# Kernel optimization log

Measured on AMD Instinct MI355X. Metric: run time of the kernel, lower is better.

The kernel has to match this reference:

```python
import jax, jax.numpy as jnp
import numpy as np

B, NL, C, H, W = 4, 2048, 128, 128, 128
N_PTS0, N_PTS1 = 32, 8
SCALE = N_PTS0 // N_PTS1  # MaxPool1d kernel/stride
FEATURE_DIM = 5
BN_EPS = 1e-5


def setup_inputs() -> dict:
    key = jax.random.key(0)
    ks = jax.random.split(key, 12)
    fm = jax.random.normal(ks[0], (B, C, H, W), dtype=jnp.float32)
    lines = jax.random.uniform(ks[1], (B, NL, 2, 2), dtype=jnp.float32) * 128.0
    P = C // 2
    s = 0.05
    return {
        "feature_map": fm,
        "lines": lines,
        # Bottleneck1D params (BatchNorm in eval mode: running_mean=0, running_var=1)
        "bn1_g": jnp.ones((C,), jnp.float32), "bn1_b": jnp.zeros((C,), jnp.float32),
        "conv1_w": jax.random.normal(ks[2], (P, C, 1), jnp.float32) * s,
        "conv1_b": jnp.zeros((P,), jnp.float32),
        "bn2_g": jnp.ones((P,), jnp.float32), "bn2_b": jnp.zeros((P,), jnp.float32),
        "conv2_w": jax.random.normal(ks[3], (P, P, 3), jnp.float32) * s,
        "conv2_b": jnp.zeros((P,), jnp.float32),
        "bn3_g": jnp.ones((P,), jnp.float32), "bn3_b": jnp.zeros((P,), jnp.float32),
        "conv3_w": jax.random.normal(ks[4], (C, P, 1), jnp.float32) * s,
        "conv3_b": jnp.zeros((C,), jnp.float32),
        # fc2: ReLU -> Linear(dim_loi*n_pts1 + 5, 4)
        "fc2_w": jax.random.normal(ks[5], (4, C * N_PTS1 + FEATURE_DIM), jnp.float32) * s,
        "fc2_b": jnp.zeros((4,), jnp.float32),
    }


def _bn(x, g, b):
    # eval-mode BatchNorm1d with running_mean=0, running_var=1
    return x * (g / jnp.sqrt(1.0 + BN_EPS))[None, :, None] + b[None, :, None]


def _conv1d(x, w, b, pad):
    y = jax.lax.conv_general_dilated(x, w, (1,), [(pad, pad)],
                                     dimension_numbers=("NCH", "OIH", "NCH"))
    return y + b[None, :, None]


def _loi_gather(fm, lines):
    # sample points along each line: [B, NL, N_PTS0, 2]
    lam = jnp.linspace(0.0, 1.0, N_PTS0, dtype=jnp.float32)[None, None, :, None]
    p = lines[:, :, 0:1, :] * lam + lines[:, :, 1:2, :] * (1.0 - lam) - 0.5
    p = p.reshape(B, -1, 2)                      # [B, NL*N_PTS0, 2]
    px, py = p[..., 0], p[..., 1]
    px0 = jnp.clip(jnp.floor(px), 0.0, 127.0)
    py0 = jnp.clip(jnp.floor(py), 0.0, 127.0)
    px1 = jnp.clip(px0 + 1.0, 0.0, 127.0)
    py1 = jnp.clip(py0 + 1.0, 0.0, 127.0)
    px0l, py0l = px0.astype(jnp.int32), py0.astype(jnp.int32)
    px1l, py1l = px1.astype(jnp.int32), py1.astype(jnp.int32)

    gather = jax.vmap(lambda f, yi, xi: f[:, yi, xi])  # [C, P] per image
    # weights exactly as in the torch source
    xp = (gather(fm, py0l, px0l) * ((px1 - px) * (py1 - py))[:, None, :]
          + gather(fm, py1l, px0l) * ((px - px0) * (py1 - py))[:, None, :]
          + gather(fm, py0l, px1l) * ((px1 - px) * (py - py0))[:, None, :]
          + gather(fm, py1l, px1l) * ((px - px0) * (py - py0))[:, None, :])
    # [B, C, NL*N_PTS0] -> [B*NL, C, N_PTS0]
    xp = xp.reshape(B, C, NL, N_PTS0).transpose(0, 2, 1, 3).reshape(B * NL, C, N_PTS0)
    return xp


def reference(feature_map, lines, bn1_g, bn1_b, conv1_w, conv1_b,
              bn2_g, bn2_b, conv2_w, conv2_b, bn3_g, bn3_b,
              conv3_w, conv3_b, fc2_w, fc2_b):
    xp = _loi_gather(feature_map, lines)               # [B*NL, C, N_PTS0]
    # MaxPool1d(SCALE, SCALE)
    x = xp.reshape(B * NL, C, N_PTS1, SCALE).max(axis=-1)
    # Bottleneck1D residual block
    y = jax.nn.relu(_bn(x, bn1_g, bn1_b))
    y = _conv1d(y, conv1_w, conv1_b, 0)
    y = jax.nn.relu(_bn(y, bn2_g, bn2_b))
    y = _conv1d(y, conv2_w, conv2_b, 1)
    y = jax.nn.relu(_bn(y, bn3_g, bn3_b))
    y = _conv1d(y, conv3_w, conv3_b, 0)
    x = x + y                                          # [B*NL, C, N_PTS1]
    # line geometry feature (use_cood=1, use_slop=1)
    xyu, xyv = lines[:, :, 0, :], lines[:, :, 1, :]
    u2v = jnp.sqrt(((xyu - xyv) ** 2).sum(-1, keepdims=True)).clip(min=1e-6)
    f = jnp.concatenate([xyu / 128.0, xyv / 128.0, u2v], axis=-1)
    f = f.reshape(B * NL, FEATURE_DIM)
    # concat + fc2 (ReLU -> Linear)
    x = jnp.concatenate([x.reshape(B * NL, C * N_PTS1), f], axis=1)
    logits = jax.nn.relu(x) @ fc2_w.T + fc2_b
    prob = jax.nn.softmax(logits, axis=1)
    return logits, prob
```

## Files before the change

kernel.cpp:

```cpp
#include <hip/hip_runtime.h>
#include <math.h>

#define BB 4
#define NLL 2048
#define CC 128
#define HH 128
#define WW 128
#define NPTS0 32
#define NPTS1 8
#define PP 64
#define FDIM 5
#define FCK (CC*NPTS1 + FDIM)
#define FCKP 1032

typedef __attribute__((ext_vector_type(8))) short bf16x8;
typedef __attribute__((ext_vector_type(4))) float f32x4;

__device__ __forceinline__ unsigned short f2bf(float f) {
    union { float f; unsigned u; } v; v.f = f;
    unsigned u = v.u;
    return (unsigned short)((u + 0x7fffu + ((u >> 16) & 1u)) >> 16);
}
__device__ __forceinline__ float bf2f(unsigned short s) {
    union { unsigned u; float f; } v; v.u = ((unsigned)s) << 16;
    return v.f;
}

__global__ __launch_bounds__(256)
void transpose_prep(const float* __restrict__ fm, const float* __restrict__ w1,
                    const float* __restrict__ w2, const float* __restrict__ w3,
                    const float* __restrict__ fcw,
                    unsigned short* __restrict__ fmT,
                    unsigned short* __restrict__ W1b,
                    unsigned short* __restrict__ W2b,
                    unsigned short* __restrict__ W3b,
                    float* __restrict__ fcwP) {
    const int t = threadIdx.x;
    if (blockIdx.x >= 512) {
        int gid = (blockIdx.x - 512) * 256 + t;
        for (int e = gid; e < 32800; e += 4096) {
            if (e < 8192) {
                W1b[e] = f2bf(w1[e]);
            } else if (e < 20480) {
                int g = e - 8192;
                int tt = g >> 12, r = g & 4095;
                int p = r >> 6, q = r & 63;
                W2b[tt * 4096 + p * 64 + q] = f2bf(w2[p * 192 + q * 3 + tt]);
            } else if (e < 28672) {
                int g = e - 20480;
                W3b[g] = f2bf(w3[g]);
            } else {
                int g = e - 28672;
                int o = g / FCKP, r = g - o * FCKP;
                fcwP[g] = (r < FCK) ? fcw[o * FCK + r] : 0.0f;
            }
        }
        return;
    }
    __shared__ unsigned short tile[2][128 * 72];
    const int by = blockIdx.x;
    const int b = by >> 7, y = by & 127;
    const float* src = fm + ((size_t)b * CC) * (HH * WW) + (size_t)y * WW;
    const int x4 = (t & 31) * 4;
    const int xh = x4 >> 6, xl = x4 & 63;
    #pragma unroll
    for (int i = 0; i < 16; ++i) {
        int r = (t >> 5) + 8 * i;
        float4 v = *(const float4*)&src[(size_t)r * (HH * WW) + x4];
        ushort4 u;
        u.x = f2bf(v.x); u.y = f2bf(v.y); u.z = f2bf(v.z); u.w = f2bf(v.w);
        *(ushort4*)&tile[xh][r * 72 + (xl ^ (r & 28))] = u;
    }
    __syncthreads();
    const int c4 = (t & 31) * 4;
    #pragma unroll
    for (int h = 0; h < 2; ++h) {
        unsigned short* dst = fmT + ((size_t)by * WW + h * 64) * CC;
        #pragma unroll
        for (int i = 0; i < 8; ++i) {
            int x = (t >> 5) + 8 * i;
            ushort4 u;
            u.x = tile[h][(c4 + 0) * 72 + (x ^ ((c4 + 0) & 28))];
            u.y = tile[h][(c4 + 1) * 72 + (x ^ ((c4 + 1) & 28))];
            u.z = tile[h][(c4 + 2) * 72 + (x ^ ((c4 + 2) & 28))];
            u.w = tile[h][(c4 + 3) * 72 + (x ^ ((c4 + 3) & 28))];
            *(ushort4*)&dst[(size_t)x * CC + c4] = u;
        }
    }
}

__global__ __launch_bounds__(256, 6)
void line_mfma(const unsigned short* __restrict__ fmT,
               const float* __restrict__ lines,
               const float* __restrict__ bn1_g, const float* __restrict__ bn1_b,
               const unsigned short* __restrict__ W1b, const float* __restrict__ b1,
               const float* __restrict__ bn2_g, const float* __restrict__ bn2_b,
               const unsigned short* __restrict__ W2b, const float* __restrict__ b2,
               const float* __restrict__ bn3_g, const float* __restrict__ bn3_b,
               const unsigned short* __restrict__ W3b, const float* __restrict__ b3,
               const float* __restrict__ fcwP,  const float* __restrict__ fcb,
               float* __restrict__ out) {
    __shared__ unsigned short s_xs[32 * 136];
    __shared__ unsigned short s_z1[4 * 10 * 72];
    __shared__ unsigned short s_z2[32 * 72];
    __shared__ float s_red[4 * 8];

    const int bx  = blockIdx.x;
    const int L0  = bx * 4;
    const int b   = bx >> 9;
    const int tid = threadIdx.x;
    const int lane = tid & 63;
    const int wv   = tid >> 6;
    const int quad = lane >> 4;
    const int l16  = lane & 15;
    const float inv_s = 1.0f / sqrtf(1.0f + 1e-5f);

    {
        int m = tid >> 3;
        int line = m >> 3, k = m & 7;
        int c16 = (tid & 7) * 16;
        const float* ln = lines + (size_t)(L0 + line) * 4;
        float lx0 = ln[0], ly0 = ln[1], lx1 = ln[2], ly1 = ln[3];
        const unsigned short* base = fmT + (size_t)b * (HH * WW * CC) + c16;
        float acc[16];
        #pragma unroll
        for (int i = 0; i < 16; ++i) acc[i] = -INFINITY;
        #pragma unroll
        for (int j = 0; j < 4; ++j) {
            int pt = k * 4 + j;
            float lam = (float)pt * (1.0f / 31.0f);
            float om  = 1.0f - lam;
            float px = lx0 * lam + lx1 * om - 0.5f;
            float py = ly0 * lam + ly1 * om - 0.5f;
            float px0 = fminf(fmaxf(floorf(px), 0.0f), 127.0f);
            float py0 = fminf(fmaxf(floorf(py), 0.0f), 127.0f);
            float px1 = fminf(px0 + 1.0f, 127.0f);
            float py1 = fminf(py0 + 1.0f, 127.0f);
            int ix0 = (int)px0, ix1 = (int)px1, iy0 = (int)py0, iy1 = (int)py1;
            float ax = px1 - px, bxv = px - px0, ay = py1 - py, byv = py - py0;
            float wA = ax * ay, wB = bxv * ay, wC = ax * byv, wD = bxv * byv;
            int oA = (iy0 * WW + ix0) * CC, oB = (iy1 * WW + ix0) * CC;
            int oC = (iy0 * WW + ix1) * CC, oD = (iy1 * WW + ix1) * CC;
            bf16x8 a0 = *(const bf16x8*)(base + oA);
            bf16x8 a1 = *(const bf16x8*)(base + oA + 8);
            bf16x8 b0 = *(const bf16x8*)(base + oB);
            bf16x8 b1v = *(const bf16x8*)(base + oB + 8);
            bf16x8 c0 = *(const bf16x8*)(base + oC);
            bf16x8 c1 = *(const bf16x8*)(base + oC + 8);
            bf16x8 d0 = *(const bf16x8*)(base + oD);
            bf16x8 d1 = *(const bf16x8*)(base + oD + 8);
            #pragma unroll
            for (int i = 0; i < 8; ++i) {
                float v = wA * bf2f((unsigned short)a0[i])
                        + wB * bf2f((unsigned short)b0[i])
                        + wC * bf2f((unsigned short)c0[i])
                        + wD * bf2f((unsigned short)d0[i]);
                acc[i] = fmaxf(acc[i], v);
                float v2 = wA * bf2f((unsigned short)a1[i])
                         + wB * bf2f((unsigned short)b1v[i])
                         + wC * bf2f((unsigned short)c1[i])
                         + wD * bf2f((unsigned short)d1[i]);
                acc[8 + i] = fmaxf(acc[8 + i], v2);
            }
        }
        bf16x8 lo, hi;
        #pragma unroll
        for (int i = 0; i < 8; ++i) {
            lo[i] = (short)f2bf(acc[i]);
            hi[i] = (short)f2bf(acc[8 + i]);
        }
        *(bf16x8*)&s_xs[m * 136 + c16]     = lo;
        *(bf16x8*)&s_xs[m * 136 + c16 + 8] = hi;
    }
    __syncthreads();

    {
        int mh = wv & 1, nh = wv >> 1;
        int mrow = mh * 16 + l16;
        bf16x8 afr[4];
        #pragma unroll
        for (int kc = 0; kc < 4; ++kc) {
            bf16x8 x = *(const bf16x8*)&s_xs[mrow * 136 + kc * 32 + quad * 8];
            int c0 = kc * 32 + quad * 8;
            float4 g0 = *(const float4*)(bn1_g + c0);
            float4 g1 = *(const float4*)(bn1_g + c0 + 4);
            float4 bb0 = *(const float4*)(bn1_b + c0);
            float4 bb1 = *(const float4*)(bn1_b + c0 + 4);
            float gs[8] = {g0.x, g0.y, g0.z, g0.w, g1.x, g1.y, g1.z, g1.w};
            float bs[8] = {bb0.x, bb0.y, bb0.z, bb0.w, bb1.x, bb1.y, bb1.z, bb1.w};
            bf16x8 pk;
            #pragma unroll
            for (int i = 0; i < 8; ++i) {
                float v = fmaxf(bf2f((unsigned short)x[i]) * (gs[i] * inv_s) + bs[i], 0.0f);
                pk[i] = (short)f2bf(v);
            }
            afr[kc] = pk;
        }
        #pragma unroll
        for (int sub = 0; sub < 2; ++sub) {
            int p = nh * 32 + sub * 16 + l16;
            f32x4 acc = {0.f, 0.f, 0.f, 0.f};
            #pragma unroll
            for (int kc = 0; kc < 4; ++kc) {
                bf16x8 bf = *(const bf16x8*)(W1b + p * 128 + kc * 32 + quad * 8);
                acc = __builtin_amdgcn_mfma_f32_16x16x32_bf16(afr[kc], bf, acc, 0, 0, 0);
            }
            float s2 = bn2_g[p] * inv_s, bb2 = bn2_b[p], cb = b1[p];
            #pragma unroll
            for (int r = 0; r < 4; ++r) {
                int mm = mh * 16 + quad * 4 + r;
                int lline = mm >> 3, kk = mm & 7;
                float v = fmaxf((acc[r] + cb) * s2 + bb2, 0.0f);
                s_z1[lline * 720 + (kk + 1) * 72 + p] = f2bf(v);
            }
        }
        #pragma unroll
        for (int e = tid; e < 512; e += 256) {
            int lline = e >> 7;
            int rr = (e >> 6) & 1;
            int q = e & 63;
            s_z1[lline * 720 + (rr ? 9 : 0) * 72 + q] = 0;
        }
    }
    __syncthreads();

    {
        int mh = wv & 1, nh = wv >> 1;
        int mrow = mh * 16 + l16;
        int linea = mrow >> 3, ka = mrow & 7;
        const unsigned short* arow = s_z1 + linea * 720 + ka * 72;
        bf16x8 afr[3][2];
        #pragma unroll
        for (int t = 0; t < 3; ++t)
            #pragma unroll
            for (int kc = 0; kc < 2; ++kc)
                afr[t][kc] = *(const bf16x8*)&arow[t * 72 + kc * 32 + quad * 8];
        #pragma unroll
        for (int sub = 0; sub < 2; ++sub) {
            int p = nh * 32 + sub * 16 + l16;
            f32x4 acc = {0.f, 0.f, 0.f, 0.f};
            #pragma unroll
            for (int t = 0; t < 3; ++t) {
                #pragma unroll
                for (int kc = 0; kc < 2; ++kc) {
                    bf16x8 bf = *(const bf16x8*)(W2b + t * 4096 + p * 64 + kc * 32 + quad * 8);
                    acc = __builtin_amdgcn_mfma_f32_16x16x32_bf16(afr[t][kc], bf, acc, 0, 0, 0);
                }
            }
            float s3 = bn3_g[p] * inv_s, bb3 = bn3_b[p], cb = b2[p];
            #pragma unroll
            for (int r = 0; r < 4; ++r) {
                int mm = mh * 16 + quad * 4 + r;
                float v = fmaxf((acc[r] + cb) * s3 + bb3, 0.0f);
                s_z2[mm * 72 + p] = f2bf(v);
            }
        }
    }
    __syncthreads();

    float p0 = 0.f, p1 = 0.f, p2 = 0.f, p3 = 0.f;
    {
        int mh = wv & 1;
        int n0 = (wv >> 1) * 64;
        int mrow = mh * 16 + l16;
        bf16x8 a0 = *(const bf16x8*)&s_z2[mrow * 72 + quad * 8];
        bf16x8 a1 = *(const bf16x8*)&s_z2[mrow * 72 + 32 + quad * 8];
        int kbase = (quad & 1) * 4;
        #pragma unroll
        for (int sub = 0; sub < 4; ++sub) {
            int c = n0 + sub * 16 + l16;
            f32x4 acc = {0.f, 0.f, 0.f, 0.f};
            bf16x8 bf0 = *(const bf16x8*)(W3b + c * 64 + quad * 8);
            bf16x8 bf1 = *(const bf16x8*)(W3b + c * 64 + 32 + quad * 8);
            acc = __builtin_amdgcn_mfma_f32_16x16x32_bf16(a0, bf0, acc, 0, 0, 0);
            acc = __builtin_amdgcn_mfma_f32_16x16x32_bf16(a1, bf1, acc, 0, 0, 0);
            float cb = b3[c];
            int idx = c * 8 + kbase;
            float4 w0 = *(const float4*)(fcwP + 0 * FCKP + idx);
            float4 w1v = *(const float4*)(fcwP + 1 * FCKP + idx);
            float4 w2v = *(const float4*)(fcwP + 2 * FCKP + idx);
            float4 w3v = *(const float4*)(fcwP + 3 * FCKP + idx);
            const float* w0a = (const float*)&w0;
            const float* w1a = (const float*)&w1v;
            const float* w2a = (const float*)&w2v;
            const float* w3a = (const float*)&w3v;
            #pragma unroll
            for (int r = 0; r < 4; ++r) {
                int mm = mh * 16 + quad * 4 + r;
                float xv = bf2f(s_xs[mm * 136 + c]);
                float v = fmaxf(xv + acc[r] + cb, 0.0f);
                p0 = fmaf(v, w0a[r], p0);
                p1 = fmaf(v, w1a[r], p1);
                p2 = fmaf(v, w2a[r], p2);
                p3 = fmaf(v, w3a[r], p3);
            }
        }
    }
    #pragma unroll
    for (int off = 16; off >= 1; off >>= 1) {
        p0 += __shfl_down(p0, off);
        p1 += __shfl_down(p1, off);
        p2 += __shfl_down(p2, off);
        p3 += __shfl_down(p3, off);
    }
    if ((lane & 31) == 0) {
        int h = lane >> 5;
        s_red[wv * 8 + h * 4 + 0] = p0;
        s_red[wv * 8 + h * 4 + 1] = p1;
        s_red[wv * 8 + h * 4 + 2] = p2;
        s_red[wv * 8 + h * 4 + 3] = p3;
    }
    __syncthreads();

    if (tid < 4) {
        int line = tid;
        int wa = line >> 1;
        int h  = (line & 1) * 4;
        float lg[4];
        #pragma unroll
        for (int o = 0; o < 4; ++o)
            lg[o] = fcb[o] + s_red[wa * 8 + h + o] + s_red[(wa + 2) * 8 + h + o];
        const float* ln = lines + (size_t)(L0 + line) * 4;
        float ux = ln[0], uy = ln[1], vx = ln[2], vy = ln[3];
        float dx = ux - vx, dy = uy - vy;
        float d = fmaxf(sqrtf(dx * dx + dy * dy), 1e-6f);
        float ft[FDIM] = {ux * (1.0f / 128.0f), uy * (1.0f / 128.0f),
                          vx * (1.0f / 128.0f), vy * (1.0f / 128.0f), d};
        #pragma unroll
        for (int j = 0; j < FDIM; ++j) {
            float fv = fmaxf(ft[j], 0.0f);
            #pragma unroll
            for (int o = 0; o < 4; ++o)
                lg[o] = fmaf(fv, fcwP[o * FCKP + 1024 + j], lg[o]);
        }
        float m = fmaxf(fmaxf(lg[0], lg[1]), fmaxf(lg[2], lg[3]));
        float e0 = expf(lg[0] - m), e1 = expf(lg[1] - m);
        float e2 = expf(lg[2] - m), e3 = expf(lg[3] - m);
        float inv = 1.0f / (e0 + e1 + e2 + e3);
        float* lo = out + (size_t)(L0 + line) * 4;
        lo[0] = lg[0]; lo[1] = lg[1]; lo[2] = lg[2]; lo[3] = lg[3];
        float* pr = out + (size_t)BB * NLL * 4 + (size_t)(L0 + line) * 4;
        pr[0] = e0 * inv; pr[1] = e1 * inv; pr[2] = e2 * inv; pr[3] = e3 * inv;
    }
}

__global__ __launch_bounds__(256)
void transpose_fm2(const float* __restrict__ fm, float* __restrict__ fmT) {
    __shared__ float tile[32 * 132];
    const int c0 = blockIdx.x * 32;
    const int by = blockIdx.y;
    const int b = by >> 7, y = by & 127;
    const int t = threadIdx.x;
    const float* src = fm + ((size_t)b * CC) * (HH * WW) + (size_t)y * WW;
    const int x4 = (t & 31) * 4;
    #pragma unroll
    for (int i = 0; i < 4; ++i) {
        int r = (t >> 5) + 8 * i;
        *(float4*)&tile[r * 132 + x4] =
            *(const float4*)&src[(size_t)(c0 + r) * (HH * WW) + x4];
    }
    __syncthreads();
    float* dst = fmT + (size_t)by * WW * CC + c0 + (t & 31);
    const int cr = (t & 31) * 132;
    #pragma unroll
    for (int i = 0; i < 16; ++i) {
        int x = (t >> 5) + 8 * i;
        dst[(size_t)x * CC] = tile[cr + x];
    }
}

template<bool TRANS>
__global__ __launch_bounds__(256)
void line_kernel_v1(const float* __restrict__ fm,
                    const float* __restrict__ lines,
                    const float* __restrict__ bn1_g, const float* __restrict__ bn1_b,
                    const float* __restrict__ w1,    const float* __restrict__ b1,
                    const float* __restrict__ bn2_g, const float* __restrict__ bn2_b,
                    const float* __restrict__ w2,    const float* __restrict__ b2,
                    const float* __restrict__ bn3_g, const float* __restrict__ bn3_b,
                    const float* __restrict__ w3,    const float* __restrict__ b3,
                    const float* __restrict__ fcw,   const float* __restrict__ fcb,
                    float* __restrict__ out) {
    __shared__ int   s_ix0[32], s_ix1[32], s_iy0[32], s_iy1[32];
    __shared__ float s_wA[32], s_wB[32], s_wC[32], s_wD[32];
    __shared__ float xs [8][132];
    __shared__ float ybn[8][132];
    __shared__ float z1 [64][12];
    __shared__ float z2 [64][8];
    __shared__ float s_feat[8];
    __shared__ float s_red[16];

    const int L   = blockIdx.x;
    const int b   = L / NLL;
    const int tid = threadIdx.x;
    const float inv_s = 1.0f / sqrtf(1.0f + 1e-5f);
    const float* ln = lines + (size_t)L * 4;

    if (tid < 32) {
        float lam = (float)tid * (1.0f / 31.0f);
        float om  = 1.0f - lam;
        float px = ln[0] * lam + ln[2] * om - 0.5f;
        float py = ln[1] * lam + ln[3] * om - 0.5f;
        float px0 = fminf(fmaxf(floorf(px), 0.0f), 127.0f);
        float py0 = fminf(fmaxf(floorf(py), 0.0f), 127.0f);
        float px1 = fminf(px0 + 1.0f, 127.0f);
        float py1 = fminf(py0 + 1.0f, 127.0f);
        s_ix0[tid] = (int)px0; s_ix1[tid] = (int)px1;
        s_iy0[tid] = (int)py0; s_iy1[tid] = (int)py1;
        float ax = px1 - px, bxv = px - px0, ay = py1 - py, byv = py - py0;
        s_wA[tid] = ax  * ay;  s_wB[tid] = bxv * ay;
        s_wC[tid] = ax  * byv; s_wD[tid] = bxv * byv;
    }
    if (tid == 0) {
        float ux = ln[0], uy = ln[1], vx = ln[2], vy = ln[3];
        float dx = ux - vx, dy = uy - vy;
        float d = fmaxf(sqrtf(dx * dx + dy * dy), 1e-6f);
        s_feat[0] = ux / 128.0f; s_feat[1] = uy / 128.0f;
        s_feat[2] = vx / 128.0f; s_feat[3] = vy / 128.0f;
        s_feat[4] = d;
    }
    __syncthreads();
    {
        int cq = tid & 31, k = tid >> 5, c0 = cq * 4;
        float4 acc;
        acc.x = -INFINITY; acc.y = -INFINITY; acc.z = -INFINITY; acc.w = -INFINITY;
        #pragma unroll
        for (int j = 0; j < 4; ++j) {
            int pt = k * 4 + j;
            int ix0 = s_ix0[pt], ix1 = s_ix1[pt];
            int iy0 = s_iy0[pt], iy1 = s_iy1[pt];
            float wA = s_wA[pt], wB = s_wB[pt], wC = s_wC[pt], wD = s_wD[pt];
            float4 vA, vB, vC, vD;
            if (TRANS) {
                const float* base = fm + (size_t)b * HH * WW * CC;
                vA = *(const float4*)(base + ((size_t)(iy0 * WW + ix0)) * CC + c0);
                vB = *(const float4*)(base + ((size_t)(iy1 * WW + ix0)) * CC + c0);
                vC = *(const float4*)(base + ((size_t)(iy0 * WW + ix1)) * CC + c0);
                vD = *(const float4*)(base + ((size_t)(iy1 * WW + ix1)) * CC + c0);
            } else {
                const float* base = fm + ((size_t)b * CC + c0) * HH * WW;
                int oA = iy0 * WW + ix0, oB = iy1 * WW + ix0;
                int oC = iy0 * WW + ix1, oD = iy1 * WW + ix1;
                vA.x = base[oA];           vB.x = base[oB];
                vC.x = base[oC];           vD.x = base[oD];
                vA.y = base[HH*WW + oA];   vB.y = base[HH*WW + oB];
                vC.y = base[HH*WW + oC];   vD.y = base[HH*WW + oD];
                vA.z = base[2*HH*WW + oA]; vB.z = base[2*HH*WW + oB];
                vC.z = base[2*HH*WW + oC]; vD.z = base[2*HH*WW + oD];
                vA.w = base[3*HH*WW + oA]; vB.w = base[3*HH*WW + oB];
                vC.w = base[3*HH*WW + oC]; vD.w = base[3*HH*WW + oD];
            }
            float4 v;
            v.x = wA * vA.x + wB * vB.x + wC * vC.x + wD * vD.x;
            v.y = wA * vA.y + wB * vB.y + wC * vC.y + wD * vD.y;
            v.z = wA * vA.z + wB * vB.z + wC * vC.z + wD * vD.z;
            v.w = wA * vA.w + wB * vB.w + wC * vC.w + wD * vD.w;
            acc.x = fmaxf(acc.x, v.x); acc.y = fmaxf(acc.y, v.y);
            acc.z = fmaxf(acc.z, v.z); acc.w = fmaxf(acc.w, v.w);
        }
        *(float4*)(&xs[k][c0]) = acc;
    }
    __syncthreads();
    for (int e = tid; e < 1024; e += 256) {
        int k = e >> 7, c = e & 127;
        ybn[k][c] = fmaxf(xs[k][c] * (bn1_g[c] * inv_s) + bn1_b[c], 0.0f);
    }
    __syncthreads();
    if (tid < 64) { z1[tid][0] = 0.0f; z1[tid][9] = 0.0f; }
    {
        int p = tid >> 2, kq = tid & 3;
        const float* wrow = w1 + p * 128;
        float a0a = 0.f, a0b = 0.f, a1a = 0.f, a1b = 0.f;
        #pragma unroll 8
        for (int c = 0; c < 128; c += 4) {
            float4 w  = *(const float4*)(wrow + c);
            float4 ya = *(const float4*)(&ybn[kq][c]);
            float4 yb = *(const float4*)(&ybn[kq + 4][c]);
            a0a = fmaf(w.x, ya.x, a0a); a0b = fmaf(w.y, ya.y, a0b);
            a0a = fmaf(w.z, ya.z, a0a); a0b = fmaf(w.w, ya.w, a0b);
            a1a = fmaf(w.x, yb.x, a1a); a1b = fmaf(w.y, yb.y, a1b);
            a1a = fmaf(w.z, yb.z, a1a); a1b = fmaf(w.w, yb.w, a1b);
        }
        float s2 = bn2_g[p] * inv_s, bb = bn2_b[p], cb = b1[p];
        z1[p][1 + kq]     = fmaxf((a0a + a0b + cb) * s2 + bb, 0.0f);
        z1[p][1 + kq + 4] = fmaxf((a1a + a1b + cb) * s2 + bb, 0.0f);
    }
    __syncthreads();
    {
        int p = tid >> 2, kq = tid & 3;
        const float* wrow = w2 + p * 192;
        float acc0 = 0.f, acc1 = 0.f;
        #pragma unroll 4
        for (int q = 0; q < 64; ++q) {
            float w0 = wrow[q * 3 + 0], w1v = wrow[q * 3 + 1], w2v = wrow[q * 3 + 2];
            const float* zr = &z1[q][0];
            acc0 = fmaf(w0, zr[kq], acc0);
            acc0 = fmaf(w1v, zr[kq + 1], acc0);
            acc0 = fmaf(w2v, zr[kq + 2], acc0);
            acc1 = fmaf(w0, zr[kq + 4], acc1);
            acc1 = fmaf(w1v, zr[kq + 5], acc1);
            acc1 = fmaf(w2v, zr[kq + 6], acc1);
        }
        float s3 = bn3_g[p] * inv_s, bb = bn3_b[p], cb = b2[p];
        z2[p][kq]     = fmaxf((acc0 + cb) * s3 + bb, 0.0f);
        z2[p][kq + 4] = fmaxf((acc1 + cb) * s3 + bb, 0.0f);
    }
    __syncthreads();
    float part0 = 0.f, part1 = 0.f, part2 = 0.f, part3 = 0.f;
    {
        int c = tid >> 1, kq = tid & 1;
        const float* wrow = w3 + c * 64;
        float acc[4] = {0.f, 0.f, 0.f, 0.f};
        #pragma unroll 8
        for (int q = 0; q < 64; ++q) {
            float w = wrow[q];
            acc[0] = fmaf(w, z2[q][kq], acc[0]);
            acc[1] = fmaf(w, z2[q][kq + 2], acc[1]);
            acc[2] = fmaf(w, z2[q][kq + 4], acc[2]);
            acc[3] = fmaf(w, z2[q][kq + 6], acc[3]);
        }
        float cb = b3[c];
        #pragma unroll
        for (int i = 0; i < 4; ++i) {
            int k = kq + 2 * i;
            float v = fmaxf(xs[k][c] + acc[i] + cb, 0.0f);
            int idx = c * 8 + k;
            part0 = fmaf(v, fcw[0 * FCK + idx], part0);
            part1 = fmaf(v, fcw[1 * FCK + idx], part1);
            part2 = fmaf(v, fcw[2 * FCK + idx], part2);
            part3 = fmaf(v, fcw[3 * FCK + idx], part3);
        }
    }
    #pragma unroll
    for (int off = 32; off > 0; off >>= 1) {
        part0 += __shfl_down(part0, off);
        part1 += __shfl_down(part1, off);
        part2 += __shfl_down(part2, off);
        part3 += __shfl_down(part3, off);
    }
    if ((tid & 63) == 0) {
        int w = tid >> 6;
        s_red[w * 4 + 0] = part0; s_red[w * 4 + 1] = part1;
        s_red[w * 4 + 2] = part2; s_red[w * 4 + 3] = part3;
    }
    __syncthreads();
    if (tid == 0) {
        float lg[4];
        #pragma unroll
        for (int o = 0; o < 4; ++o)
            lg[o] = fcb[o] + s_red[o] + s_red[4 + o] + s_red[8 + o] + s_red[12 + o];
        #pragma unroll
        for (int j = 0; j < FDIM; ++j) {
            float fv = fmaxf(s_feat[j], 0.0f);
            #pragma unroll
            for (int o = 0; o < 4; ++o)
                lg[o] = fmaf(fv, fcw[o * FCK + 1024 + j], lg[o]);
        }
        float m = fmaxf(fmaxf(lg[0], lg[1]), fmaxf(lg[2], lg[3]));
        float e0 = expf(lg[0] - m), e1 = expf(lg[1] - m);
        float e2 = expf(lg[2] - m), e3 = expf(lg[3] - m);
        float inv = 1.0f / (e0 + e1 + e2 + e3);
        float* lo = out + (size_t)L * 4;
        lo[0] = lg[0]; lo[1] = lg[1]; lo[2] = lg[2]; lo[3] = lg[3];
        float* pr = out + (size_t)BB * NLL * 4 + (size_t)L * 4;
        pr[0] = e0 * inv; pr[1] = e1 * inv; pr[2] = e2 * inv; pr[3] = e3 * inv;
    }
}

extern "C" void kernel_launch(void* const* d_in, const int* in_sizes, int n_in,
                              void* d_out, int out_size, void* d_ws, size_t ws_size,
                              hipStream_t stream) {
    const float* fm     = (const float*)d_in[0];
    const float* lines  = (const float*)d_in[1];
    const float* bn1_g  = (const float*)d_in[2];
    const float* bn1_b  = (const float*)d_in[3];
    const float* w1     = (const float*)d_in[4];
    const float* b1     = (const float*)d_in[5];
    const float* bn2_g  = (const float*)d_in[6];
    const float* bn2_b  = (const float*)d_in[7];
    const float* w2     = (const float*)d_in[8];
    const float* b2     = (const float*)d_in[9];
    const float* bn3_g  = (const float*)d_in[10];
    const float* bn3_b  = (const float*)d_in[11];
    const float* w3     = (const float*)d_in[12];
    const float* b3     = (const float*)d_in[13];
    const float* fcw    = (const float*)d_in[14];
    const float* fcb    = (const float*)d_in[15];
    float* out = (float*)d_out;

    const size_t fmTb_bytes = (size_t)BB * HH * WW * CC * sizeof(unsigned short);
    const size_t fmTf_bytes = (size_t)BB * HH * WW * CC * sizeof(float);
    const size_t wb_bytes   = 57344;
    const size_t fcwP_bytes = 4 * FCKP * sizeof(float);

    if (ws_size >= fmTb_bytes + wb_bytes + fcwP_bytes) {
        unsigned short* fmT = (unsigned short*)d_ws;
        unsigned short* W1b = (unsigned short*)((char*)d_ws + fmTb_bytes);
        unsigned short* W2b = W1b + 8192;
        unsigned short* W3b = W2b + 12288;
        float* fcwP = (float*)((char*)d_ws + fmTb_bytes + wb_bytes);
        transpose_prep<<<512 + 16, 256, 0, stream>>>(
            fm, w1, w2, w3, fcw, fmT, W1b, W2b, W3b, fcwP);
        line_mfma<<<BB * NLL / 4, 256, 0, stream>>>(
            fmT, lines, bn1_g, bn1_b, W1b, b1, bn2_g, bn2_b, W2b, b2,
            bn3_g, bn3_b, W3b, b3, fcwP, fcb, out);
    } else if (ws_size >= fmTf_bytes) {
        float* fmT = (float*)d_ws;
        dim3 tg(CC / 32, BB * HH);
        transpose_fm2<<<tg, 256, 0, stream>>>(fm, fmT);
        line_kernel_v1<true><<<BB * NLL, 256, 0, stream>>>(
            fmT, lines, bn1_g, bn1_b, w1, b1, bn2_g, bn2_b, w2, b2,
            bn3_g, bn3_b, w3, b3, fcw, fcb, out);
    } else {
        line_kernel_v1<false><<<BB * NLL, 256, 0, stream>>>(
            fm, lines, bn1_g, bn1_b, w1, b1, bn2_g, bn2_b, w2, b2,
            bn3_g, bn3_b, w3, b3, fcw, fcb, out);
    }
}
```

Baseline: 177.1 us.

## Precompute bilinear offsets in LDS, halve gather width, alias shared buffers for occupancy

The first 128 threads compute bilinear corner offsets and weights once per sample point and store them in shared memory. Every thread then gathers 8 channels per pass over two passes, instead of 16 channels with all coordinate math repeated. The shared buffers are packed into one aliased byte array, and the launch bound goes from 6 to 8 blocks per CU. The aim is lower register pressure and higher occupancy, hiding gather latency better. In exchange it adds an extra barrier and LDS traffic, and it serializes the gather into two passes.

```diff
diff --git a/kernel.cpp b/kernel.cpp
--- a/kernel.cpp
+++ b/kernel.cpp
@@ -89,7 +89,7 @@
     }
 }
 
-__global__ __launch_bounds__(256, 6)
+__global__ __launch_bounds__(256, 8)
 void line_mfma(const unsigned short* __restrict__ fmT,
                const float* __restrict__ lines,
                const float* __restrict__ bn1_g, const float* __restrict__ bn1_b,
@@ -100,10 +100,19 @@
                const unsigned short* __restrict__ W3b, const float* __restrict__ b3,
                const float* __restrict__ fcwP,  const float* __restrict__ fcb,
                float* __restrict__ out) {
-    __shared__ unsigned short s_xs[32 * 136];
-    __shared__ unsigned short s_z1[4 * 10 * 72];
-    __shared__ unsigned short s_z2[32 * 72];
-    __shared__ float s_red[4 * 8];
+    __shared__ __align__(16) char smem[19200];
+    int*   s_oA = (int*)(smem + 0);
+    int*   s_oB = (int*)(smem + 512);
+    int*   s_oC = (int*)(smem + 1024);
+    int*   s_oD = (int*)(smem + 1536);
+    float* s_wA = (float*)(smem + 2048);
+    float* s_wB = (float*)(smem + 2560);
+    float* s_wC = (float*)(smem + 3072);
+    float* s_wD = (float*)(smem + 3584);
+    unsigned short* s_z1 = (unsigned short*)(smem + 0);
+    unsigned short* s_xs = (unsigned short*)(smem + 5760);
+    unsigned short* s_z2 = (unsigned short*)(smem + 14464);
+    float* s_red = (float*)(smem + 19072);
 
     const int bx  = blockIdx.x;
     const int L0  = bx * 4;
@@ -115,62 +124,60 @@
     const int l16  = lane & 15;
     const float inv_s = 1.0f / sqrtf(1.0f + 1e-5f);
 
-    {
-        int m = tid >> 3;
+    if (tid < 128) {
+        int line = tid >> 5, pt = tid & 31;
+        const float* ln = lines + (size_t)(L0 + line) * 4;
+        float lam = (float)pt * (1.0f / 31.0f);
+        float om  = 1.0f - lam;
+        float px = ln[0] * lam + ln[2] * om - 0.5f;
+        float py = ln[1] * lam + ln[3] * om - 0.5f;
+        float px0 = fminf(fmaxf(floorf(px), 0.0f), 127.0f);
+        float py0 = fminf(fmaxf(floorf(py), 0.0f), 127.0f);
+        float px1 = fminf(px0 + 1.0f, 127.0f);
+        float py1 = fminf(py0 + 1.0f, 127.0f);
+        int ix0 = (int)px0, ix1 = (int)px1, iy0 = (int)py0, iy1 = (int)py1;
+        s_oA[tid] = (iy0 * WW + ix0) * CC;
+        s_oB[tid] = (iy1 * WW + ix0) * CC;
+        s_oC[tid] = (iy0 * WW + ix1) * CC;
+        s_oD[tid] = (iy1 * WW + ix1) * CC;
+        float ax = px1 - px, bxv = px - px0, ay = py1 - py, byv = py - py0;
+        s_wA[tid] = ax  * ay;
+        s_wB[tid] = bxv * ay;
+        s_wC[tid] = ax  * byv;
+        s_wD[tid] = bxv * byv;
+    }
+    __syncthreads();
+
+    #pragma unroll 1
+    for (int h = 0; h < 2; ++h) {
+        int m = h * 16 + (tid >> 4);
         int line = m >> 3, k = m & 7;
-        int c16 = (tid & 7) * 16;
-        const float* ln = lines + (size_t)(L0 + line) * 4;
-        float lx0 = ln[0], ly0 = ln[1], lx1 = ln[2], ly1 = ln[3];
-        const unsigned short* base = fmT + (size_t)b * (HH * WW * CC) + c16;
-        float acc[16];
-        #pragma unroll
-        for (int i = 0; i < 16; ++i) acc[i] = -INFINITY;
+        int c8 = (tid & 15) * 8;
+        const unsigned short* base = fmT + (size_t)b * (HH * WW * CC) + c8;
+        float acc[8];
+        #pragma unroll
+        for (int i = 0; i < 8; ++i) acc[i] = -INFINITY;
         #pragma unroll
         for (int j = 0; j < 4; ++j) {
-            int pt = k * 4 + j;
-            float lam = (float)pt * (1.0f / 31.0f);
-            float om  = 1.0f - lam;
-            float px = lx0 * lam + lx1 * om - 0.5f;
-            float py = ly0 * lam + ly1 * om - 0.5f;
-            float px0 = fminf(fmaxf(floorf(px), 0.0f), 127.0f);
-            float py0 = fminf(fmaxf(floorf(py), 0.0f), 127.0f);
-            float px1 = fminf(px0 + 1.0f, 127.0f);
-            float py1 = fminf(py0 + 1.0f, 127.0f);
-            int ix0 = (int)px0, ix1 = (int)px1, iy0 = (int)py0, iy1 = (int)py1;
-            float ax = px1 - px, bxv = px - px0, ay = py1 - py, byv = py - py0;
-            float wA = ax * ay, wB = bxv * ay, wC = ax * byv, wD = bxv * byv;
-            int oA = (iy0 * WW + ix0) * CC, oB = (iy1 * WW + ix0) * CC;
-            int oC = (iy0 * WW + ix1) * CC, oD = (iy1 * WW + ix1) * CC;
-            bf16x8 a0 = *(const bf16x8*)(base + oA);
-            bf16x8 a1 = *(const bf16x8*)(base + oA + 8);
-            bf16x8 b0 = *(const bf16x8*)(base + oB);
-            bf16x8 b1v = *(const bf16x8*)(base + oB + 8);
-            bf16x8 c0 = *(const bf16x8*)(base + oC);
-            bf16x8 c1 = *(const bf16x8*)(base + oC + 8);
-            bf16x8 d0 = *(const bf16x8*)(base + oD);
-            bf16x8 d1 = *(const bf16x8*)(base + oD + 8);
+            int pt = line * 32 + k * 4 + j;
+            bf16x8 rA = *(const bf16x8*)(base + s_oA[pt]);
+            bf16x8 rB = *(const bf16x8*)(base + s_oB[pt]);
+            bf16x8 rC = *(const bf16x8*)(base + s_oC[pt]);
+            bf16x8 rD = *(const bf16x8*)(base + s_oD[pt]);
+            float wA = s_wA[pt], wB = s_wB[pt], wC = s_wC[pt], wD = s_wD[pt];
             #pragma unroll
             for (int i = 0; i < 8; ++i) {
-                float v = wA * bf2f((unsigned short)a0[i])
-                        + wB * bf2f((unsigned short)b0[i])
-                        + wC * bf2f((unsigned short)c0[i])
-                        + wD * bf2f((unsigned short)d0[i]);
+                float v = wA * bf2f((unsigned short)rA[i])
+                        + wB * bf2f((unsigned short)rB[i])
+                        + wC * bf2f((unsigned short)rC[i])
+                        + wD * bf2f((unsigned short)rD[i]);
                 acc[i] = fmaxf(acc[i], v);
-                float v2 = wA * bf2f((unsigned short)a1[i])
-                         + wB * bf2f((unsigned short)b1v[i])
-                         + wC * bf2f((unsigned short)c1[i])
-                         + wD * bf2f((unsigned short)d1[i]);
-                acc[8 + i] = fmaxf(acc[8 + i], v2);
-            }
-        }
-        bf16x8 lo, hi;
-        #pragma unroll
-        for (int i = 0; i < 8; ++i) {
-            lo[i] = (short)f2bf(acc[i]);
-            hi[i] = (short)f2bf(acc[8 + i]);
-        }
-        *(bf16x8*)&s_xs[m * 136 + c16]     = lo;
-        *(bf16x8*)&s_xs[m * 136 + c16 + 8] = hi;
+            }
+        }
+        bf16x8 pk;
+        #pragma unroll
+        for (int i = 0; i < 8; ++i) pk[i] = (short)f2bf(acc[i]);
+        *(bf16x8*)&s_xs[m * 136 + c8] = pk;
     }
     __syncthreads();
 
```

Result: faster. 163.6 us (-7.6%).
